# Optimization experiments

Measured on AMD Instinct MI355X. Metric: run time of the kernel, lower is better.

The kernel has to match this reference:

```python
import jax, jax.numpy as jnp
import numpy as np

B, PANO, OBJ, CFG, LM, IMG, D = 64, 36, 36, 16, 8, 32, 300
H, EMB, ANG, FEAT = 512, 64, 128, 2176
TOPN = 3
EPS = 1e-8


def setup_inputs() -> dict:
    key = jax.random.key(0)
    ks = jax.random.split(key, 24)
    f = lambda i, shape: jax.random.normal(ks[i], shape, dtype=jnp.float32)
    u = lambda i, shape: jax.random.uniform(ks[i], shape, dtype=jnp.float32)
    s = 0.02
    return {
        "action": f(0, (B, ANG)),
        "feature": f(1, (B, PANO, FEAT)),
        "cand_feat": f(2, (B, IMG, FEAT)),
        "prev_h1": f(3, (B, H)),
        "c_0": f(4, (B, H)),
        "ctx": f(5, (B, CFG, H)),
        "s_0": u(6, (B, CFG)),
        "landmark_object_feature": f(7, (B, CFG, LM, D)),
        "candidate_obj_text_feat": f(8, (B, IMG, OBJ, D)),
        "landmark_mask": u(9, (B, CFG, LM)),
        "landmark_relation": f(10, (B, CFG, LM, 6)),
        "landmark_relation_mask": u(11, (B, CFG, LM)),
        "candidate_relation": f(12, (B, IMG, 6)),
        "pano_obj_feat": f(13, (B, PANO, OBJ, D)),
        "emb_W": f(14, (ANG, EMB)) * s,
        "emb_b": jnp.zeros((EMB,), jnp.float32),
        "W_ih": f(15, (EMB + FEAT + TOPN * D, 4 * H)) * s,
        "W_hh": f(16, (H, 4 * H)) * s,
        "b_lstm": jnp.zeros((4 * H,), jnp.float32),
        "feat_in_W": f(17, (H, FEAT + TOPN * D)) * s,
        "att_in_W": f(18, (H, H)) * s,
        "att_out_W": f(19, (2 * H, H)) * s,
        "cand_in_W": f(20, (H, FEAT + TOPN * 7 + TOPN * D)) * s,
        "ctx_mask": jnp.zeros((B, CFG), dtype=bool),
    }


def _cos_argmax(obj_feat, land_flat):
    # obj_feat: [B,I,O,D], land_flat: [B,M,D] -> argmax over O of cosine sim: [B,I,M]
    dot = jnp.einsum('biod,bmd->biom', obj_feat, land_flat)
    na = jnp.linalg.norm(obj_feat, axis=-1)
    nb = jnp.linalg.norm(land_flat, axis=-1)
    sim = dot / jnp.maximum(na[..., None] * nb[:, None, None, :], EPS)
    return jnp.argmax(sim, axis=2)


def reference(action, feature, cand_feat, prev_h1, c_0, ctx, s_0,
              landmark_object_feature, candidate_obj_text_feat, landmark_mask,
              landmark_relation, landmark_relation_mask, candidate_relation,
              pano_obj_feat, emb_W, emb_b, W_ih, W_hh, b_lstm, feat_in_W,
              att_in_W, att_out_W, cand_in_W, ctx_mask):
    M = CFG * LM
    land_flat = landmark_object_feature.reshape(B, M, D)

    # --- pano object retrieval (cosine argmax + top-N config*landmark gather) ---
    pano_idx = _cos_argmax(pano_obj_feat, land_flat)                   # [B,36,M]
    top_idx = jax.lax.top_k((s_0[..., None] * landmark_mask).reshape(B, M), TOPN)[1]  # [B,3]
    sel = jnp.take_along_axis(pano_idx, jnp.broadcast_to(top_idx[:, None, :], (B, PANO, TOPN)), axis=2)
    pano_sim_obj = jnp.take_along_axis(
        pano_obj_feat, jnp.broadcast_to(sel[..., None], (B, PANO, TOPN, D)), axis=2
    ).reshape(B, PANO, TOPN * D)

    # --- embed action, feature attention (dropout = identity in eval) ---
    action_embeds = jnp.tanh(action @ emb_W + emb_b)
    feat_all = jnp.concatenate([feature, pano_sim_obj], axis=-1)       # [B,36,FEAT+900]
    a = jnp.einsum('bsd,bd->bs', feat_all, prev_h1 @ feat_in_W)
    p = jax.nn.softmax(a, axis=-1)
    attn_feat = jnp.einsum('bs,bsd->bd', p, feat_all)

    # --- LSTM cell ---
    gates = jnp.concatenate([action_embeds, attn_feat], axis=-1) @ W_ih + prev_h1 @ W_hh + b_lstm
    i_g, f_g, g_g, o_g = jnp.split(gates, 4, axis=-1)
    c_1 = jax.nn.sigmoid(f_g) * c_0 + jax.nn.sigmoid(i_g) * jnp.tanh(g_g)
    h_1 = jax.nn.sigmoid(o_g) * jnp.tanh(c_1)

    # --- ctx attention with mask + tilde ---
    lg = jnp.einsum('bsd,bd->bs', ctx, h_1 @ att_in_W)
    lg = jnp.where(ctx_mask, -jnp.inf, lg)
    ctx_attn = jax.nn.softmax(lg, axis=-1)
    wctx = jnp.einsum('bs,bsd->bd', ctx_attn, ctx)
    h_tilde = jnp.tanh(jnp.concatenate([wctx, h_1], axis=-1) @ att_out_W)

    # --- candidate object retrieval ---
    cand_idx = _cos_argmax(candidate_obj_text_feat, land_flat)         # [B,IMG,M]
    ctop = jax.lax.top_k((ctx_attn[..., None] * landmark_mask).reshape(B, M), TOPN)[1]
    land_rel_top = jnp.take_along_axis(landmark_relation.reshape(B, M, 6),
                                       jnp.broadcast_to(ctop[..., None], (B, TOPN, 6)), axis=1)
    land_obj_rel = jnp.einsum('bik,bjk->bij', candidate_relation, land_rel_top)   # [B,IMG,3]
    rel_mask_top = jnp.take_along_axis(landmark_relation_mask.reshape(B, M), ctop, axis=1)  # [B,3]
    csel = jnp.take_along_axis(cand_idx, jnp.broadcast_to(ctop[:, None, :], (B, IMG, TOPN)), axis=2)
    candi_sim_obj = jnp.take_along_axis(
        candidate_obj_text_feat, jnp.broadcast_to(csel[..., None], (B, IMG, TOPN, D)), axis=2)
    candi_rel = candidate_relation[:, :, None, :] * rel_mask_top[:, None, :, None]  # [B,IMG,3,6]
    new_feat = jnp.concatenate(
        [candi_sim_obj, jnp.concatenate([candi_rel, land_obj_rel[..., None]], axis=-1)],
        axis=-1).reshape(B, IMG, TOPN * (D + 7))
    cand_all = jnp.concatenate([cand_feat, new_feat], axis=-1)

    logit = jnp.einsum('bsd,bd->bs', cand_all, h_tilde @ cand_in_W)
    return h_1, c_1, logit, h_tilde, ctx_attn
```

## Files before the change

### kernel.cpp

```cpp
#include <hip/hip_runtime.h>
#include <math.h>

#define B_    64
#define PANO_ 36
#define OBJ_  36
#define CFG_  16
#define LM_   8
#define IMG_  32
#define D_    300
#define H_    512
#define EMB_  64
#define ANG_  128
#define FEAT_ 2176
#define M_    128

__device__ __forceinline__ float sigmoidf(float x) { return 1.0f / (1.0f + expf(-x)); }
__device__ __forceinline__ float dot4(float4 a, float4 b) {
    return a.x * b.x + a.y * b.y + a.z * b.z + a.w * b.w;
}
__device__ __forceinline__ float4 add4(float4 a, float4 b) {
    return make_float4(a.x + b.x, a.y + b.y, a.z + b.z, a.w + b.w);
}
__device__ __forceinline__ float4 fma4(float s, float4 a, float4 acc) {
    return make_float4(acc.x + s * a.x, acc.y + s * a.y, acc.z + s * a.z, acc.w + s * a.w);
}
__device__ __forceinline__ float4 ld4(const float* p) { return *reinterpret_cast<const float4*>(p); }

template <int TWO_SEG, int VEC_B>
__global__ __launch_bounds__(256)
void gemm_part(const float* __restrict__ A0, int lda0, int K0, const float* __restrict__ W0,
               const float* __restrict__ A1, int lda1, int K1, const float* __restrict__ W1,
               float* __restrict__ part, int N, int kchunk) {
    __shared__ __align__(16) float As[64][36];
    __shared__ __align__(16) float Bs[32][68];
    const int K = K0 + (TWO_SEG ? K1 : 0);
    int n0 = blockIdx.x * 64;
    int k0 = blockIdx.y * kchunk;
    if (k0 >= K) return;
    int kend = min(K, k0 + kchunk);
    int tid = threadIdx.x;
    int tr = tid >> 4, tc = tid & 15;
    float4 rA4[2];
    float4 rB4[2];
    float rB[8];
    float acc[4][4] = {};

    auto loadA = [&](int kb) {
#pragma unroll
        for (int l = 0; l < 2; l++) {
            int idx = tid + 256 * l;
            int r = idx >> 3, kq = idx & 7;
            int k = kb + 4 * kq;
            float4 v = make_float4(0.f, 0.f, 0.f, 0.f);
            if (k < kend) {
                const float* src = (TWO_SEG && k >= K0)
                    ? A1 + (size_t)r * lda1 + (k - K0)
                    : A0 + (size_t)r * lda0 + k;
                v = ld4(src);
            }
            rA4[l] = v;
        }
    };
    auto loadB = [&](int kb) {
        if (VEC_B) {
#pragma unroll
            for (int l = 0; l < 2; l++) {
                int idx = tid + 256 * l;
                int kk = idx >> 4, c4 = idx & 15;
                int k = kb + kk, n = n0 + 4 * c4;
                float4 v = make_float4(0.f, 0.f, 0.f, 0.f);
                if (k < kend && n < N) {
                    const float* src = (TWO_SEG && k >= K0)
                        ? W1 + (size_t)(k - K0) * N + n
                        : W0 + (size_t)k * N + n;
                    v = ld4(src);
                }
                rB4[l] = v;
            }
        } else {
#pragma unroll
            for (int l = 0; l < 8; l++) {
                int idx = tid + 256 * l;
                int kk = idx >> 6, c = idx & 63;
                int k = kb + kk, n = n0 + c;
                float v = 0.f;
                if (k < kend && n < N) {
                    v = (TWO_SEG && k >= K0) ? W1[(size_t)(k - K0) * N + n]
                                             : W0[(size_t)k * N + n];
                }
                rB[l] = v;
            }
        }
    };
    auto storeLDS = [&]() {
#pragma unroll
        for (int l = 0; l < 2; l++) {
            int idx = tid + 256 * l;
            *reinterpret_cast<float4*>(&As[idx >> 3][4 * (idx & 7)]) = rA4[l];
        }
        if (VEC_B) {
#pragma unroll
            for (int l = 0; l < 2; l++) {
                int idx = tid + 256 * l;
                *reinterpret_cast<float4*>(&Bs[idx >> 4][4 * (idx & 15)]) = rB4[l];
            }
        } else {
#pragma unroll
            for (int l = 0; l < 8; l++) {
                int idx = tid + 256 * l;
                Bs[idx >> 6][idx & 63] = rB[l];
            }
        }
    };
    auto compute = [&]() {
#pragma unroll
        for (int kk0 = 0; kk0 < 32; kk0 += 4) {
            float4 a0 = ld4(&As[4 * tr + 0][kk0]);
            float4 a1 = ld4(&As[4 * tr + 1][kk0]);
            float4 a2 = ld4(&As[4 * tr + 2][kk0]);
            float4 a3 = ld4(&As[4 * tr + 3][kk0]);
            float4 b0 = ld4(&Bs[kk0 + 0][4 * tc]);
            float4 b1 = ld4(&Bs[kk0 + 1][4 * tc]);
            float4 b2 = ld4(&Bs[kk0 + 2][4 * tc]);
            float4 b3 = ld4(&Bs[kk0 + 3][4 * tc]);
#define ROWFMA(i, ai) \
            acc[i][0] += ai.x * b0.x + ai.y * b1.x + ai.z * b2.x + ai.w * b3.x; \
            acc[i][1] += ai.x * b0.y + ai.y * b1.y + ai.z * b2.y + ai.w * b3.y; \
            acc[i][2] += ai.x * b0.z + ai.y * b1.z + ai.z * b2.z + ai.w * b3.z; \
            acc[i][3] += ai.x * b0.w + ai.y * b1.w + ai.z * b2.w + ai.w * b3.w;
            ROWFMA(0, a0) ROWFMA(1, a1) ROWFMA(2, a2) ROWFMA(3, a3)
#undef ROWFMA
        }
    };

    loadA(k0); loadB(k0);
    storeLDS();
    __syncthreads();
    for (int kb = k0 + 32; kb < kend; kb += 32) {
        loadA(kb); loadB(kb);
        compute();
        __syncthreads();
        storeLDS();
        __syncthreads();
    }
    compute();

    float* outp = part + (size_t)blockIdx.y * 64 * N;
    if (VEC_B) {
#pragma unroll
        for (int i = 0; i < 4; i++) {
            int r = 4 * tr + i;
            int n = n0 + 4 * tc;
            if (n < N)
                *reinterpret_cast<float4*>(outp + (size_t)r * N + n) =
                    make_float4(acc[i][0], acc[i][1], acc[i][2], acc[i][3]);
        }
    } else {
#pragma unroll
        for (int i = 0; i < 4; i++) {
            int r = 4 * tr + i;
#pragma unroll
            for (int j = 0; j < 4; j++) {
                int n = n0 + 4 * tc + j;
                if (n < N) outp[(size_t)r * N + n] = acc[i][j];
            }
        }
    }
}

__global__ void reduce4_top3_kernel(const float4* __restrict__ part, int S, int total4,
                                    float4* __restrict__ out,
                                    const float* __restrict__ s0,
                                    const float* __restrict__ lmask,
                                    int* __restrict__ pmids) {
    int tid = threadIdx.x;
    if (blockIdx.x < 193) {
        int i = blockIdx.x * 256 + tid;
        if (i >= total4) return;
        float4 v = make_float4(0.f, 0.f, 0.f, 0.f);
        for (int s = 0; s < S; s++) v = add4(v, part[(size_t)s * total4 + i]);
        out[i] = v;
        return;
    }
    __shared__ float redV[2];
    __shared__ int redI[2];
    __shared__ int mids[3];
    int b = blockIdx.x - 193;
    int wave = tid >> 6, lane = tid & 63;
    float tv; int tm;
    if (tid < 128) { tv = s0[b * CFG_ + (tid >> 3)] * lmask[(size_t)b * M_ + tid]; tm = tid; }
    else { tv = -INFINITY; tm = 1 << 30; }
    for (int t = 0; t < 3; t++) {
        float bv = tv; int bi = tm;
        for (int off = 32; off >= 1; off >>= 1) {
            float ov = __shfl_xor(bv, off);
            int   oi = __shfl_xor(bi, off);
            if (ov > bv || (ov == bv && oi < bi)) { bv = ov; bi = oi; }
        }
        if (lane == 0 && wave < 2) { redV[wave] = bv; redI[wave] = bi; }
        __syncthreads();
        if (tid == 0) {
            int pick = (redV[0] > redV[1] || (redV[0] == redV[1] && redI[0] < redI[1])) ? redI[0] : redI[1];
            mids[t] = pick;
            pmids[b * 3 + t] = pick;
        }
        __syncthreads();
        if (tm == mids[t]) tv = -INFINITY;
    }
}

__global__ void reduce_remap_kernel(const float* __restrict__ part, int S,
                                    float* __restrict__ out) {
    int b = blockIdx.y;
    int c = blockIdx.x * 256 + threadIdx.x;
    if (c >= 3097) return;
    float v = 0.f;
    for (int s = 0; s < S; s++) v += part[(size_t)s * (B_ * 3097) + (size_t)b * 3097 + c];
    int oc;
    if (c < 2176) oc = c;
    else { int u = c - 2176; oc = 2176 + (u / 307) * 308 + (u % 307); }
    out[(size_t)b * 3104 + oc] = v;
}

__global__ void tanh_reduce_kernel(const float4* __restrict__ part, int S,
                                   float4* __restrict__ htld, float4* __restrict__ out_ht) {
    int i = blockIdx.x * 256 + threadIdx.x;
    if (i >= B_ * H_ / 4) return;
    float4 v = make_float4(0.f, 0.f, 0.f, 0.f);
    for (int s = 0; s < S; s++) v = add4(v, part[(size_t)s * (B_ * H_ / 4) + i]);
    float4 t = make_float4(tanhf(v.x), tanhf(v.y), tanhf(v.z), tanhf(v.w));
    htld[i] = t;
    out_ht[i] = t;
}

__device__ __forceinline__ void stage_tile_batched(const float* __restrict__ obase,
                                                   float tile[36][308], int tid) {
    float4 v[11];
#pragma unroll
    for (int j = 0; j < 11; j++) {
        int q = tid + 256 * j;
        if (q < 2700) v[j] = ld4(obase + 4 * q);
    }
#pragma unroll
    for (int j = 0; j < 11; j++) {
        int q = tid + 256 * j;
        if (q < 2700)
            *reinterpret_cast<float4*>(&tile[q / 75][4 * (q % 75)]) = v[j];
    }
}

__global__ __launch_bounds__(256)
void pano_logits_kernel(const float* __restrict__ pobj,
                        const float* __restrict__ land,
                        const int* __restrict__ pmids,
                        const float* __restrict__ feature,
                        const float* __restrict__ qfeat,
                        int* __restrict__ sel,
                        float* __restrict__ aval) {
    __shared__ __align__(16) float tile[36][308];
    __shared__ __align__(16) float land3[3][304];
    __shared__ int mids[3];
    __shared__ float simv[3][40];
    __shared__ int fin[3];
    __shared__ float wred[4];
    int i = blockIdx.x, b = blockIdx.y, tid = threadIdx.x;
    int wave = tid >> 6, lane = tid & 63;

    if (tid < 3) mids[tid] = pmids[b * 3 + tid];
    __syncthreads();

    if (tid < 225) {
        int t = tid / 75, k4 = tid % 75;
        *reinterpret_cast<float4*>(&land3[t][4 * k4]) =
            ld4(land + ((size_t)b * 128 + mids[t]) * 300 + 4 * k4);
    }
    const float* obase = pobj + (((size_t)b * 36 + i) * 36) * 300;
    stage_tile_batched(obase, tile, tid);
    __syncthreads();

    int g = tid >> 2, gl = tid & 3;
    if (g < 36) {
        float c0 = 0, c1 = 0, c2 = 0, sn = 0;
        for (int k4 = gl; k4 < 75; k4 += 4) {
            float4 a = ld4(&tile[g][4 * k4]);
            sn += dot4(a, a);
            c0 += dot4(a, ld4(&land3[0][4 * k4]));
            c1 += dot4(a, ld4(&land3[1][4 * k4]));
            c2 += dot4(a, ld4(&land3[2][4 * k4]));
        }
#pragma unroll
        for (int off = 1; off <= 2; off <<= 1) {
            c0 += __shfl_xor(c0, off);
            c1 += __shfl_xor(c1, off);
            c2 += __shfl_xor(c2, off);
            sn += __shfl_xor(sn, off);
        }
        if (gl == 0) {
            float inv = 1.0f / sqrtf(fmaxf(sn, 1e-20f));
            simv[0][g] = c0 * inv;
            simv[1][g] = c1 * inv;
            simv[2][g] = c2 * inv;
        }
    }
    __syncthreads();
    if (tid < 3) {
        float bv = -INFINITY; int bo = 0;
        for (int o2 = 0; o2 < 36; o2++) {
            float v = simv[tid][o2];
            if (v > bv) { bv = v; bo = o2; }
        }
        fin[tid] = bo;
        sel[((size_t)b * 36 + i) * 3 + tid] = bo;
    }
    __syncthreads();

    const float* qf = qfeat + (size_t)b * 3076;
    const float* frow = feature + ((size_t)b * 36 + i) * 2176;
    float acc = 0;
#pragma unroll
    for (int j = 0; j < 3; j++) {
        int d4 = tid + 256 * j;
        if (d4 < 544)
            acc += dot4(ld4(frow + 4 * d4), ld4(qf + 4 * d4));
    }
    if (tid < 225) {
        int t = tid / 75, k4 = tid % 75;
        acc += dot4(ld4(&tile[fin[t]][4 * k4]), ld4(qf + 2176 + t * 300 + 4 * k4));
    }
    for (int off = 32; off >= 1; off >>= 1) acc += __shfl_xor(acc, off);
    if (lane == 0) wred[wave] = acc;
    __syncthreads();
    if (tid == 0) aval[b * 36 + i] = wred[0] + wred[1] + wred[2] + wred[3];
}

__global__ __launch_bounds__(256)
void attn_wsum_kernel(const float* __restrict__ feature,
                      const float* __restrict__ pobj,
                      const int* __restrict__ sel,
                      const float* __restrict__ aval,
                      const float* __restrict__ action,
                      const float* __restrict__ embW,
                      const float* __restrict__ embB,
                      float* __restrict__ xcat) {
    __shared__ float lg[36];
    __shared__ float pe[36];
    __shared__ int ss[36][3];
    int b = blockIdx.y, tid = threadIdx.x;
    int d4 = blockIdx.x * 256 + tid;
    if (tid < 36) lg[tid] = aval[b * 36 + tid];
    for (int idx = tid; idx < 108; idx += 256) ss[idx / 3][idx % 3] = sel[(size_t)b * 108 + idx];
    __syncthreads();
    float mx = -INFINITY;
    for (int s = 0; s < 36; s++) mx = fmaxf(mx, lg[s]);
    if (tid < 36) pe[tid] = expf(lg[tid] - mx);
    __syncthreads();
    float sum = 0;
    for (int s = 0; s < 36; s++) sum += pe[s];
    float invS = 1.0f / sum;
    if (d4 < 769) {
        float4 acc = make_float4(0.f, 0.f, 0.f, 0.f);
        if (d4 < 544) {
            const float* fb = feature + (size_t)b * 36 * 2176 + 4 * d4;
#pragma unroll 4
            for (int s = 0; s < 36; s++) acc = fma4(pe[s], ld4(fb + (size_t)s * 2176), acc);
        } else {
            int u = d4 - 544, t = u / 75, k4 = u % 75;
            const float* pb = pobj + (size_t)b * 36 * 36 * 300;
#pragma unroll 4
            for (int s = 0; s < 36; s++)
                acc = fma4(pe[s], ld4(pb + ((size_t)s * 36 + ss[s][t]) * 300 + 4 * k4), acc);
        }
        acc = make_float4(acc.x * invS, acc.y * invS, acc.z * invS, acc.w * invS);
        *reinterpret_cast<float4*>(xcat + (size_t)b * 3140 + 64 + 4 * d4) = acc;
    }
    if (blockIdx.x == 0 && tid < 64) {
        float acc = embB[tid];
        for (int k = 0; k < ANG_; k++)
            acc += action[b * ANG_ + k] * embW[k * EMB_ + tid];
        xcat[(size_t)b * 3140 + tid] = tanhf(acc);
    }
}

__global__ void lstm_kernel(const float* __restrict__ gp, int S,
                            const float* __restrict__ b_lstm,
                            const float* __restrict__ c0,
                            float* __restrict__ out_h1,
                            float* __restrict__ out_c1) {
    int idx4 = blockIdx.x * 256 + threadIdx.x;
    if (idx4 >= B_ * H_ / 4) return;
    int b = idx4 >> 7;
    int d4 = idx4 & 127;
    float4 ig = ld4(b_lstm + 4 * d4);
    float4 fg = ld4(b_lstm + 512 + 4 * d4);
    float4 gg = ld4(b_lstm + 1024 + 4 * d4);
    float4 og = ld4(b_lstm + 1536 + 4 * d4);
    for (int s = 0; s < S; s++) {
        const float* g = gp + (size_t)s * (B_ * 2048) + (size_t)b * 2048 + 4 * d4;
        ig = add4(ig, ld4(g));
        fg = add4(fg, ld4(g + 512));
        gg = add4(gg, ld4(g + 1024));
        og = add4(og, ld4(g + 1536));
    }
    float4 cv = ld4(c0 + 4 * idx4);
    float4 c1, h1;
    c1.x = sigmoidf(fg.x) * cv.x + sigmoidf(ig.x) * tanhf(gg.x);
    c1.y = sigmoidf(fg.y) * cv.y + sigmoidf(ig.y) * tanhf(gg.y);
    c1.z = sigmoidf(fg.z) * cv.z + sigmoidf(ig.z) * tanhf(gg.z);
    c1.w = sigmoidf(fg.w) * cv.w + sigmoidf(ig.w) * tanhf(gg.w);
    h1.x = sigmoidf(og.x) * tanhf(c1.x);
    h1.y = sigmoidf(og.y) * tanhf(c1.y);
    h1.z = sigmoidf(og.z) * tanhf(c1.z);
    h1.w = sigmoidf(og.w) * tanhf(c1.w);
    *reinterpret_cast<float4*>(out_c1 + 4 * idx4) = c1;
    *reinterpret_cast<float4*>(out_h1 + 4 * idx4) = h1;
}

__global__ __launch_bounds__(256)
void ctx_attn_kernel(const float* __restrict__ ctx,
                     const float* __restrict__ qctx_part,
                     const float* __restrict__ h1f,
                     const float* __restrict__ lmask,
                     float* __restrict__ ccbuf,
                     float* __restrict__ out_attn,
                     int* __restrict__ ctop) {
    __shared__ __align__(16) float qc[512];
    __shared__ float part[16][17];
    __shared__ float lgv[16];
    __shared__ float att[16];
    __shared__ float redV[2];
    __shared__ int redI[2];
    __shared__ int mids[3];
    int b = blockIdx.x, tid = threadIdx.x;
    int wave = tid >> 6, lane = tid & 63;
    if (tid < 128) {
        float4 v = make_float4(0.f, 0.f, 0.f, 0.f);
#pragma unroll
        for (int s = 0; s < 8; s++)
            v = add4(v, ld4(qctx_part + (size_t)s * (B_ * 512) + (size_t)b * 512 + 4 * tid));
        *reinterpret_cast<float4*>(&qc[4 * tid]) = v;
    }
    __syncthreads();
    int s = tid >> 4, l = tid & 15;
    float acc = 0;
    for (int d = l; d < 512; d += 16) acc += ctx[((size_t)b * 16 + s) * 512 + d] * qc[d];
    part[s][l] = acc;
    __syncthreads();
    if (tid < 16) {
        float sum = 0;
        for (int j = 0; j < 16; j++) sum += part[tid][j];
        lgv[tid] = sum;
    }
    __syncthreads();
    if (tid < 16) {
        float mx = -INFINITY;
        for (int j = 0; j < 16; j++) mx = fmaxf(mx, lgv[j]);
        att[tid] = expf(lgv[tid] - mx);
    }
    __syncthreads();
    float sum = 0;
    for (int j = 0; j < 16; j++) sum += att[j];
    float invS = 1.0f / sum;
    if (tid < 16) out_attn[b * 16 + tid] = att[tid] * invS;
    for (int d = tid; d < 512; d += 256) {
        float acc2 = 0;
        for (int sj = 0; sj < 16; sj++)
            acc2 += att[sj] * ctx[((size_t)b * 16 + sj) * 512 + d];
        ccbuf[(size_t)b * 1024 + d] = acc2 * invS;
        ccbuf[(size_t)b * 1024 + 512 + d] = h1f[(size_t)b * 512 + d];
    }
    float tv; int tm;
    if (tid < 128) { tv = att[tid >> 3] * lmask[(size_t)b * M_ + tid]; tm = tid; }
    else { tv = -INFINITY; tm = 1 << 30; }
    for (int t = 0; t < 3; t++) {
        float bv = tv; int bi = tm;
        for (int off = 32; off >= 1; off >>= 1) {
            float ov = __shfl_xor(bv, off);
            int   oi = __shfl_xor(bi, off);
            if (ov > bv || (ov == bv && oi < bi)) { bv = ov; bi = oi; }
        }
        if (lane == 0 && wave < 2) { redV[wave] = bv; redI[wave] = bi; }
        __syncthreads();
        if (tid == 0) {
            int pick = (redV[0] > redV[1] || (redV[0] == redV[1] && redI[0] < redI[1])) ? redI[0] : redI[1];
            mids[t] = pick;
            ctop[b * 3 + t] = pick;
        }
        __syncthreads();
        if (tm == mids[t]) tv = -INFINITY;
    }
}

__global__ __launch_bounds__(256)
void cand_fused_kernel(const float* __restrict__ cobj,
                       const float* __restrict__ land,
                       const int* __restrict__ ctop,
                       const float* __restrict__ landrel,
                       const float* __restrict__ lrmask,
                       const float* __restrict__ crel_g,
                       const float* __restrict__ cand_feat,
                       const float* __restrict__ qcand,
                       float* __restrict__ out_logit) {
    __shared__ __align__(16) float tile[36][308];
    __shared__ __align__(16) float land3[3][304];
    __shared__ float relL[3][6];
    __shared__ float relM[3];
    __shared__ float crel[6];
    __shared__ int mids[3];
    __shared__ float simv[3][40];
    __shared__ int fin[3];
    __shared__ float wsum[4];
    int img = blockIdx.x, b = blockIdx.y, tid = threadIdx.x;
    int wave = tid >> 6, lane = tid & 63;
    if (tid < 3) mids[tid] = ctop[b * 3 + tid];
    __syncthreads();

    if (tid < 225) {
        int t = tid / 75, k4 = tid % 75;
        *reinterpret_cast<float4*>(&land3[t][4 * k4]) =
            ld4(land + ((size_t)b * 128 + mids[t]) * 300 + 4 * k4);
    }
    const float* obase = cobj + (((size_t)b * 32 + img) * 36) * 300;
    stage_tile_batched(obase, tile, tid);
    if (tid < 18) { int t = tid / 6, k = tid % 6; relL[t][k] = landrel[((size_t)b * 128 + mids[t]) * 6 + k]; }
    if (tid >= 32 && tid < 35) { int t = tid - 32; relM[t] = lrmask[(size_t)b * 128 + mids[t]]; }
    if (tid >= 64 && tid < 70) { crel[tid - 64] = crel_g[((size_t)b * 32 + img) * 6 + (tid - 64)]; }
    __syncthreads();

    int g = tid >> 2, gl = tid & 3;
    if (g < 36) {
        float c0 = 0, c1 = 0, c2 = 0, sn = 0;
        for (int k4 = gl; k4 < 75; k4 += 4) {
            float4 a = ld4(&tile[g][4 * k4]);
            sn += dot4(a, a);
            c0 += dot4(a, ld4(&land3[0][4 * k4]));
            c1 += dot4(a, ld4(&land3[1][4 * k4]));
            c2 += dot4(a, ld4(&land3[2][4 * k4]));
        }
#pragma unroll
        for (int off = 1; off <= 2; off <<= 1) {
            c0 += __shfl_xor(c0, off);
            c1 += __shfl_xor(c1, off);
            c2 += __shfl_xor(c2, off);
            sn += __shfl_xor(sn, off);
        }
        if (gl == 0) {
            float inv = 1.0f / sqrtf(fmaxf(sn, 1e-20f));
            simv[0][g] = c0 * inv;
            simv[1][g] = c1 * inv;
            simv[2][g] = c2 * inv;
        }
    }
    __syncthreads();
    if (tid < 3) {
        float bv = -INFINITY; int bo = 0;
        for (int o2 = 0; o2 < 36; o2++) {
            float v = simv[tid][o2];
            if (v > bv) { bv = v; bo = o2; }
        }
        fin[tid] = bo;
    }
    __syncthreads();

    const float* q = qcand + (size_t)b * 3104;
    const float* cf = cand_feat + ((size_t)b * 32 + img) * 2176;
    float acc = 0;
#pragma unroll
    for (int j = 0; j < 3; j++) {
        int d4 = tid + 256 * j;
        if (d4 < 544)
            acc += dot4(ld4(cf + 4 * d4), ld4(q + 4 * d4));
    }
    if (tid < 225) {
        int t = tid / 75, k4 = tid % 75;
        acc += dot4(ld4(&tile[fin[t]][4 * k4]), ld4(q + 2176 + t * 308 + 4 * k4));
    }
    if (tid < 21) {
        int t = tid / 7, j = tid % 7;
        float val;
        if (j < 6) val = crel[j] * relM[t];
        else { val = 0; for (int k = 0; k < 6; k++) val += crel[k] * relL[t][k]; }
        acc += val * q[2176 + t * 308 + 300 + j];
    }
    for (int off = 32; off >= 1; off >>= 1) acc += __shfl_xor(acc, off);
    if (lane == 0) wsum[wave] = acc;
    __syncthreads();
    if (tid == 0) {
        out_logit[(size_t)b * 32 + img] = wsum[0] + wsum[1] + wsum[2] + wsum[3];
    }
}

extern "C" void kernel_launch(void* const* d_in, const int* in_sizes, int n_in,
                              void* d_out, int out_size, void* d_ws, size_t ws_size,
                              hipStream_t stream) {
    const float* action    = (const float*)d_in[0];
    const float* feature   = (const float*)d_in[1];
    const float* cand_feat = (const float*)d_in[2];
    const float* prev_h1   = (const float*)d_in[3];
    const float* c_0       = (const float*)d_in[4];
    const float* ctx       = (const float*)d_in[5];
    const float* s_0       = (const float*)d_in[6];
    const float* lobj      = (const float*)d_in[7];
    const float* cobj      = (const float*)d_in[8];
    const float* lmask     = (const float*)d_in[9];
    const float* lrel      = (const float*)d_in[10];
    const float* lrelmask  = (const float*)d_in[11];
    const float* crel      = (const float*)d_in[12];
    const float* pobj      = (const float*)d_in[13];
    const float* embW      = (const float*)d_in[14];
    const float* embB      = (const float*)d_in[15];
    const float* W_ih      = (const float*)d_in[16];
    const float* W_hh      = (const float*)d_in[17];
    const float* b_lstm    = (const float*)d_in[18];
    const float* feat_in_W = (const float*)d_in[19];
    const float* att_in_W  = (const float*)d_in[20];
    const float* att_out_W = (const float*)d_in[21];
    const float* cand_in_W = (const float*)d_in[22];

    float* ws = (float*)d_ws;
    float* gates_part = ws;
    float* qf_part    = gates_part + 2621440;
    float* q_feat     = qf_part + 1574912;
    float* qctx_part  = q_feat + 196864;
    float* htpre_part = qctx_part + 262144;
    float* htld       = htpre_part + 524288;
    float* qcand_part = htld + 32768;
    float* q_cand     = qcand_part + 1585664;
    float* xcat       = q_cand + 198656;
    float* ccbuf      = xcat + 200960;
    float* aval       = ccbuf + 65536;
    int*   ctop       = (int*)(aval + 2304);
    int*   sel        = ctop + 192;
    int*   pmids      = sel + 6912;

    float* out       = (float*)d_out;
    float* out_h1    = out;
    float* out_c1    = out + 32768;
    float* out_logit = out + 65536;
    float* out_ht    = out + 67584;
    float* out_attn  = out + 100352;

    gemm_part<0, 1><<<dim3(49, 8), 256, 0, stream>>>(prev_h1, H_, H_, feat_in_W,
                                                     nullptr, 0, 0, nullptr,
                                                     qf_part, 3076, 64);
    reduce4_top3_kernel<<<257, 256, 0, stream>>>((const float4*)qf_part, 8, 49216,
                                                 (float4*)q_feat, s_0, lmask, pmids);

    pano_logits_kernel<<<dim3(PANO_, B_), 256, 0, stream>>>(pobj, lobj, pmids, feature, q_feat, sel, aval);

    attn_wsum_kernel<<<dim3(4, B_), 256, 0, stream>>>(feature, pobj, sel, aval, action, embW, embB, xcat);

    gemm_part<1, 1><<<dim3(32, 20), 256, 0, stream>>>(xcat, 3140, 3140, W_ih,
                                                      prev_h1, H_, H_, W_hh,
                                                      gates_part, 2048, 192);
    lstm_kernel<<<32, 256, 0, stream>>>(gates_part, 20, b_lstm, c_0, out_h1, out_c1);

    gemm_part<0, 1><<<dim3(8, 8), 256, 0, stream>>>(out_h1, H_, H_, att_in_W,
                                                    nullptr, 0, 0, nullptr,
                                                    qctx_part, H_, 64);
    ctx_attn_kernel<<<B_, 256, 0, stream>>>(ctx, qctx_part, out_h1, lmask, ccbuf, out_attn, ctop);

    gemm_part<0, 1><<<dim3(8, 16), 256, 0, stream>>>(ccbuf, 1024, 1024, att_out_W,
                                                     nullptr, 0, 0, nullptr,
                                                     htpre_part, H_, 64);
    tanh_reduce_kernel<<<32, 256, 0, stream>>>((const float4*)htpre_part, 16,
                                               (float4*)htld, (float4*)out_ht);

    gemm_part<0, 0><<<dim3(49, 8), 256, 0, stream>>>(htld, H_, H_, cand_in_W,
                                                     nullptr, 0, 0, nullptr,
                                                     qcand_part, 3097, 64);
    reduce_remap_kernel<<<dim3(13, B_), 256, 0, stream>>>(qcand_part, 8, q_cand);

    cand_fused_kernel<<<dim3(IMG_, B_), 256, 0, stream>>>(cobj, lobj, ctop, lrel, lrelmask,
                                                          crel, cand_feat, q_cand, out_logit);
}
```

Before: 430.5 us.

## Drop split-K for feat/cand GEMMs, fuse remap into epilogue, overlap feature dots

The two GEMMs that produce q_feat and q_cand now run without split-K (kchunk=512, a single K slice) and write their results directly, with the column remap for q_cand folded into the GEMM epilogue. This removes two reduction kernels and their partial-sum buffers. Top-3 selection moves into its own small kernel. In the pano and candidate kernels, waves 3 and up compute the feature dot product while waves 0-2 compute the cosine similarities, instead of doing the two steps one after the other. The risk is that each of the two GEMMs now launches only 49 blocks, which could leave most CUs idle and make those GEMMs slower.

```diff
diff --git a/kernel.cpp b/kernel.cpp
--- a/kernel.cpp
+++ b/kernel.cpp
@@ -26,7 +26,7 @@
 }
 __device__ __forceinline__ float4 ld4(const float* p) { return *reinterpret_cast<const float4*>(p); }
 
-template <int TWO_SEG, int VEC_B>
+template <int TWO_SEG, int VEC_B, int REMAP>
 __global__ __launch_bounds__(256)
 void gemm_part(const float* __restrict__ A0, int lda0, int K0, const float* __restrict__ W0,
                const float* __restrict__ A1, int lda1, int K1, const float* __restrict__ W1,
@@ -162,34 +162,31 @@
 #pragma unroll
             for (int j = 0; j < 4; j++) {
                 int n = n0 + 4 * tc + j;
-                if (n < N) outp[(size_t)r * N + n] = acc[i][j];
-            }
-        }
-    }
-}
-
-__global__ void reduce4_top3_kernel(const float4* __restrict__ part, int S, int total4,
-                                    float4* __restrict__ out,
-                                    const float* __restrict__ s0,
-                                    const float* __restrict__ lmask,
-                                    int* __restrict__ pmids) {
-    int tid = threadIdx.x;
-    if (blockIdx.x < 193) {
-        int i = blockIdx.x * 256 + tid;
-        if (i >= total4) return;
-        float4 v = make_float4(0.f, 0.f, 0.f, 0.f);
-        for (int s = 0; s < S; s++) v = add4(v, part[(size_t)s * total4 + i]);
-        out[i] = v;
-        return;
-    }
+                if (n < N) {
+                    if (REMAP) {
+                        int oc;
+                        if (n < 2176) oc = n;
+                        else { int u = n - 2176; oc = 2176 + (u / 307) * 308 + (u % 307); }
+                        part[(size_t)r * 3104 + oc] = acc[i][j];
+                    } else {
+                        outp[(size_t)r * N + n] = acc[i][j];
+                    }
+                }
+            }
+        }
+    }
+}
+
+__global__ void top3_kernel(const float* __restrict__ s0,
+                            const float* __restrict__ lmask,
+                            int* __restrict__ pmids) {
     __shared__ float redV[2];
     __shared__ int redI[2];
     __shared__ int mids[3];
-    int b = blockIdx.x - 193;
+    int b = blockIdx.x, tid = threadIdx.x;
     int wave = tid >> 6, lane = tid & 63;
-    float tv; int tm;
-    if (tid < 128) { tv = s0[b * CFG_ + (tid >> 3)] * lmask[(size_t)b * M_ + tid]; tm = tid; }
-    else { tv = -INFINITY; tm = 1 << 30; }
+    float tv = s0[b * CFG_ + (tid >> 3)] * lmask[(size_t)b * M_ + tid];
+    int tm = tid;
     for (int t = 0; t < 3; t++) {
         float bv = tv; int bi = tm;
         for (int off = 32; off >= 1; off >>= 1) {
@@ -197,29 +194,14 @@
             int   oi = __shfl_xor(bi, off);
             if (ov > bv || (ov == bv && oi < bi)) { bv = ov; bi = oi; }
         }
-        if (lane == 0 && wave < 2) { redV[wave] = bv; redI[wave] = bi; }
+        if (lane == 0) { redV[wave] = bv; redI[wave] = bi; }
         __syncthreads();
-        if (tid == 0) {
-            int pick = (redV[0] > redV[1] || (redV[0] == redV[1] && redI[0] < redI[1])) ? redI[0] : redI[1];
-            mids[t] = pick;
-            pmids[b * 3 + t] = pick;
-        }
+        if (tid == 0)
+            mids[t] = (redV[0] > redV[1] || (redV[0] == redV[1] && redI[0] < redI[1])) ? redI[0] : redI[1];
         __syncthreads();
+        if (tid == 0) pmids[b * 3 + t] = mids[t];
         if (tm == mids[t]) tv = -INFINITY;
     }
-}
-
-__global__ void reduce_remap_kernel(const float* __restrict__ part, int S,
-                                    float* __restrict__ out) {
-    int b = blockIdx.y;
-    int c = blockIdx.x * 256 + threadIdx.x;
-    if (c >= 3097) return;
-    float v = 0.f;
-    for (int s = 0; s < S; s++) v += part[(size_t)s * (B_ * 3097) + (size_t)b * 3097 + c];
-    int oc;
-    if (c < 2176) oc = c;
-    else { int u = c - 2176; oc = 2176 + (u / 307) * 308 + (u % 307); }
-    out[(size_t)b * 3104 + oc] = v;
 }
 
 __global__ void tanh_reduce_kernel(const float4* __restrict__ part, int S,
@@ -278,28 +260,42 @@
     stage_tile_batched(obase, tile, tid);
     __syncthreads();
 
-    int g = tid >> 2, gl = tid & 3;
-    if (g < 36) {
-        float c0 = 0, c1 = 0, c2 = 0, sn = 0;
-        for (int k4 = gl; k4 < 75; k4 += 4) {
-            float4 a = ld4(&tile[g][4 * k4]);
-            sn += dot4(a, a);
-            c0 += dot4(a, ld4(&land3[0][4 * k4]));
-            c1 += dot4(a, ld4(&land3[1][4 * k4]));
-            c2 += dot4(a, ld4(&land3[2][4 * k4]));
-        }
-#pragma unroll
-        for (int off = 1; off <= 2; off <<= 1) {
-            c0 += __shfl_xor(c0, off);
-            c1 += __shfl_xor(c1, off);
-            c2 += __shfl_xor(c2, off);
-            sn += __shfl_xor(sn, off);
-        }
-        if (gl == 0) {
-            float inv = 1.0f / sqrtf(fmaxf(sn, 1e-20f));
-            simv[0][g] = c0 * inv;
-            simv[1][g] = c1 * inv;
-            simv[2][g] = c2 * inv;
+    const float* qf = qfeat + (size_t)b * 3076;
+    const float* frow = feature + ((size_t)b * 36 + i) * 2176;
+    float facc = 0.f;
+
+    if (tid < 192) {
+        int g = tid >> 2, gl = tid & 3;
+        if (g < 36) {
+            float c0 = 0, c1 = 0, c2 = 0, sn = 0;
+            for (int k4 = gl; k4 < 75; k4 += 4) {
+                float4 a = ld4(&tile[g][4 * k4]);
+                sn += dot4(a, a);
+                c0 += dot4(a, ld4(&land3[0][4 * k4]));
+                c1 += dot4(a, ld4(&land3[1][4 * k4]));
+                c2 += dot4(a, ld4(&land3[2][4 * k4]));
+            }
+#pragma unroll
+            for (int off = 1; off <= 2; off <<= 1) {
+                c0 += __shfl_xor(c0, off);
+                c1 += __shfl_xor(c1, off);
+                c2 += __shfl_xor(c2, off);
+                sn += __shfl_xor(sn, off);
+            }
+            if (gl == 0) {
+                float inv = 1.0f / sqrtf(fmaxf(sn, 1e-20f));
+                simv[0][g] = c0 * inv;
+                simv[1][g] = c1 * inv;
+                simv[2][g] = c2 * inv;
+            }
+        }
+    } else {
+        int l = tid - 192;
+#pragma unroll
+        for (int j = 0; j < 9; j++) {
+            int d4 = l + 64 * j;
+            if (d4 < 544)
+                facc += dot4(ld4(frow + 4 * d4), ld4(qf + 4 * d4));
         }
     }
     __syncthreads();
@@ -314,15 +310,7 @@
     }
     __syncthreads();
 
-    const float* qf = qfeat + (size_t)b * 3076;
-    const float* frow = feature + ((size_t)b * 36 + i) * 2176;
-    float acc = 0;
-#pragma unroll
-    for (int j = 0; j < 3; j++) {
-        int d4 = tid + 256 * j;
-        if (d4 < 544)
-            acc += dot4(ld4(frow + 4 * d4), ld4(qf + 4 * d4));
-    }
+    float acc = facc;
     if (tid < 225) {
         int t = tid / 75, k4 = tid % 75;
         acc += dot4(ld4(&tile[fin[t]][4 * k4]), ld4(qf + 2176 + t * 300 + 4 * k4));
@@ -526,28 +514,42 @@
     if (tid >= 64 && tid < 70) { crel[tid - 64] = crel_g[((size_t)b * 32 + img) * 6 + (tid - 64)]; }
     __syncthreads();
 
-    int g = tid >> 2, gl = tid & 3;
-    if (g < 36) {
-        float c0 = 0, c1 = 0, c2 = 0, sn = 0;
-        for (int k4 = gl; k4 < 75; k4 += 4) {
-            float4 a = ld4(&tile[g][4 * k4]);
-            sn += dot4(a, a);
-            c0 += dot4(a, ld4(&land3[0][4 * k4]));
-            c1 += dot4(a, ld4(&land3[1][4 * k4]));
-            c2 += dot4(a, ld4(&land3[2][4 * k4]));
-        }
-#pragma unroll
-        for (int off = 1; off <= 2; off <<= 1) {
-            c0 += __shfl_xor(c0, off);
-            c1 += __shfl_xor(c1, off);
-            c2 += __shfl_xor(c2, off);
-            sn += __shfl_xor(sn, off);
-        }
-        if (gl == 0) {
-            float inv = 1.0f / sqrtf(fmaxf(sn, 1e-20f));
-            simv[0][g] = c0 * inv;
-            simv[1][g] = c1 * inv;
-            simv[2][g] = c2 * inv;
+    const float* q = qcand + (size_t)b * 3104;
+    const float* cf = cand_feat + ((size_t)b * 32 + img) * 2176;
+    float facc = 0.f;
+
+    if (tid < 192) {
+        int g = tid >> 2, gl = tid & 3;
+        if (g < 36) {
+            float c0 = 0, c1 = 0, c2 = 0, sn = 0;
+            for (int k4 = gl; k4 < 75; k4 += 4) {
+                float4 a = ld4(&tile[g][4 * k4]);
+                sn += dot4(a, a);
+                c0 += dot4(a, ld4(&land3[0][4 * k4]));
+                c1 += dot4(a, ld4(&land3[1][4 * k4]));
+                c2 += dot4(a, ld4(&land3[2][4 * k4]));
+            }
+#pragma unroll
+            for (int off = 1; off <= 2; off <<= 1) {
+                c0 += __shfl_xor(c0, off);
+                c1 += __shfl_xor(c1, off);
+                c2 += __shfl_xor(c2, off);
+                sn += __shfl_xor(sn, off);
+            }
+            if (gl == 0) {
+                float inv = 1.0f / sqrtf(fmaxf(sn, 1e-20f));
+                simv[0][g] = c0 * inv;
+                simv[1][g] = c1 * inv;
+                simv[2][g] = c2 * inv;
+            }
+        }
+    } else {
+        int l = tid - 192;
+#pragma unroll
+        for (int j = 0; j < 9; j++) {
+            int d4 = l + 64 * j;
+            if (d4 < 544)
+                facc += dot4(ld4(cf + 4 * d4), ld4(q + 4 * d4));
         }
     }
     __syncthreads();
@@ -561,15 +563,7 @@
     }
     __syncthreads();
 
-    const float* q = qcand + (size_t)b * 3104;
-    const float* cf = cand_feat + ((size_t)b * 32 + img) * 2176;
-    float acc = 0;
-#pragma unroll
-    for (int j = 0; j < 3; j++) {
-        int d4 = tid + 256 * j;
-        if (d4 < 544)
-            acc += dot4(ld4(cf + 4 * d4), ld4(q + 4 * d4));
-    }
+    float acc = facc;
     if (tid < 225) {
         int t = tid / 75, k4 = tid % 75;
         acc += dot4(ld4(&tile[fin[t]][4 * k4]), ld4(q + 2176 + t * 308 + 4 * k4));
@@ -618,13 +612,11 @@
 
     float* ws = (float*)d_ws;
     float* gates_part = ws;
-    float* qf_part    = gates_part + 2621440;
-    float* q_feat     = qf_part + 1574912;
-    float* qctx_part  = q_feat + 196864;
+    float* qctx_part  = gates_part + 2621440;
     float* htpre_part = qctx_part + 262144;
     float* htld       = htpre_part + 524288;
-    float* qcand_part = htld + 32768;
-    float* q_cand     = qcand_part + 1585664;
+    float* q_feat     = htld + 32768;
+    float* q_cand     = q_feat + 196864;
     float* xcat       = q_cand + 198656;
     float* ccbuf      = xcat + 200960;
     float* aval       = ccbuf + 65536;
@@ -639,36 +631,35 @@
     float* out_ht    = out + 67584;
     float* out_attn  = out + 100352;
 
-    gemm_part<0, 1><<<dim3(49, 8), 256, 0, stream>>>(prev_h1, H_, H_, feat_in_W,
-                                                     nullptr, 0, 0, nullptr,
-                                                     qf_part, 3076, 64);
-    reduce4_top3_kernel<<<257, 256, 0, stream>>>((const float4*)qf_part, 8, 49216,
-                                                 (float4*)q_feat, s_0, lmask, pmids);
+    top3_kernel<<<B_, 128, 0, stream>>>(s_0, lmask, pmids);
+
+    gemm_part<0, 1, 0><<<dim3(49, 1), 256, 0, stream>>>(prev_h1, H_, H_, feat_in_W,
+                                                        nullptr, 0, 0, nullptr,
+                                                        q_feat, 3076, 512);
 
     pano_logits_kernel<<<dim3(PANO_, B_), 256, 0, stream>>>(pobj, lobj, pmids, feature, q_feat, sel, aval);
 
     attn_wsum_kernel<<<dim3(4, B_), 256, 0, stream>>>(feature, pobj, sel, aval, action, embW, embB, xcat);
 
-    gemm_part<1, 1><<<dim3(32, 20), 256, 0, stream>>>(xcat, 3140, 3140, W_ih,
-                                                      prev_h1, H_, H_, W_hh,
-                                                      gates_part, 2048, 192);
+    gemm_part<1, 1, 0><<<dim3(32, 20), 256, 0, stream>>>(xcat, 3140, 3140, W_ih,
+                                                         prev_h1, H_, H_, W_hh,
+                                                         gates_part, 2048, 192);
     lstm_kernel<<<32, 256, 0, stream>>>(gates_part, 20, b_lstm, c_0, out_h1, out_c1);
 
-    gemm_part<0, 1><<<dim3(8, 8), 256, 0, stream>>>(out_h1, H_, H_, att_in_W,
-                                                    nullptr, 0, 0, nullptr,
-                                                    qctx_part, H_, 64);
+    gemm_part<0, 1, 0><<<dim3(8, 8), 256, 0, stream>>>(out_h1, H_, H_, att_in_W,
+                                                       nullptr, 0, 0, nullptr,
+                                                       qctx_part, H_, 64);
     ctx_attn_kernel<<<B_, 256, 0, stream>>>(ctx, qctx_part, out_h1, lmask, ccbuf, out_attn, ctop);
 
-    gemm_part<0, 1><<<dim3(8, 16), 256, 0, stream>>>(ccbuf, 1024, 1024, att_out_W,
-                                                     nullptr, 0, 0, nullptr,
-                                                     htpre_part, H_, 64);
+    gemm_part<0, 1, 0><<<dim3(8, 16), 256, 0, stream>>>(ccbuf, 1024, 1024, att_out_W,
+                                                        nullptr, 0, 0, nullptr,
+                                                        htpre_part, H_, 64);
     tanh_reduce_kernel<<<32, 256, 0, stream>>>((const float4*)htpre_part, 16,
                                                (float4*)htld, (float4*)out_ht);
 
-    gemm_part<0, 0><<<dim3(49, 8), 256, 0, stream>>>(htld, H_, H_, cand_in_W,
-                                                     nullptr, 0, 0, nullptr,
-                                                     qcand_part, 3097, 64);
-    reduce_remap_kernel<<<dim3(13, B_), 256, 0, stream>>>(qcand_part, 8, q_cand);
+    gemm_part<0, 0, 1><<<dim3(49, 1), 256, 0, stream>>>(htld, H_, H_, cand_in_W,
+                                                        nullptr, 0, 0, nullptr,
+                                                        q_cand, 3097, 512);
 
     cand_fused_kernel<<<dim3(IMG_, B_), 256, 0, stream>>>(cobj, lobj, ctop, lrel, lrelmask,
                                                           crel, cand_feat, q_cand, out_logit);
```

After: 463.1 us. 1.08x slower.
